# Kernel optimization log

Hardware: AMD Instinct MI355X
Metric: run time of the kernel (lower is better)

## Reference

```python
import jax, jax.numpy as jnp
import numpy as np

N, T, H = 307, 256, 64
NH, DH = 4, 16  # transformer heads, head dim (64/4)


def _layernorm(x, g, b, eps=1e-5):
    mu = x.mean(-1, keepdims=True)
    var = ((x - mu) ** 2).mean(-1, keepdims=True)
    return (x - mu) / jnp.sqrt(var + eps) * g + b


def _run_cell(x, m, tf, tj, Anorm, W0, b0, W1, mixW, mixb, Wih, Whh, bih, bhh, outW, outb, jamW, jamb):
    # x,m,tf,tj: [N,T]. Per-timestep 4-path ChebConv(K=2) + softmax mixing + GRUCell.
    hidden = Whh.shape[1]

    def step(h, xs):
        x_t, m_t, tf_t, tj_t = xs  # each [N]
        msg_in = jnp.concatenate([h, m_t[:, None], tf_t[:, None], tj_t[:, None]], axis=-1)  # [N,H+3]
        am = Anorm @ msg_in  # [N,H+3]
        m_all = jnp.tanh(jnp.einsum('ni,poi->npo', msg_in, W0) + b0
                         + jnp.einsum('ni,poi->npo', am, W1))  # [N,4,H]
        mix = jax.nn.softmax(h @ mixW.T + mixb, axis=1)  # [N,4]
        msg = jnp.einsum('np,npo->no', mix, m_all)  # [N,H]
        inp = jnp.concatenate([msg, (x_t * m_t)[:, None], m_t[:, None]], axis=-1)  # [N,H+2]
        # PyTorch GRUCell (gate order r,z,n)
        gi = inp @ Wih.T + bih
        gh = h @ Whh.T + bhh
        i_r, i_z, i_n = jnp.split(gi, 3, axis=-1)
        h_r, h_z, h_n = jnp.split(gh, 3, axis=-1)
        r = jax.nn.sigmoid(i_r + h_r)
        z = jax.nn.sigmoid(i_z + h_z)
        n = jnp.tanh(i_n + r * h_n)
        h_new = (1.0 - z) * n + z * h
        h2 = h_new + 0.1 * h
        pred = (h2 @ outW.T + outb)[:, 0]
        jam = (h2 @ jamW.T + jamb)[:, 0]
        return h2, (pred, jam, h2)

    h0 = jnp.zeros((x.shape[0], hidden), x.dtype)
    _, (preds, jams, hs) = jax.lax.scan(step, h0, (x.T, m.T, tf.T, tj.T))
    return preds.T, jams.T, jnp.transpose(hs, (1, 0, 2))  # [N,T],[N,T],[N,T,H]


def _pos_enc(Tlen, hdim, dtype):
    pos = jnp.arange(Tlen, dtype=dtype)[:, None]
    div = 10000.0 ** (jnp.arange(0, hdim, 2, dtype=dtype) / hdim)
    pe = jnp.zeros((Tlen, hdim), dtype)
    pe = pe.at[:, 0::2].set(jnp.sin(pos / div))
    pe = pe.at[:, 1::2].set(jnp.cos(pos / div))
    return pe


def _enhancer(h, qkvW, qkvb, oW, ob, g1, be1, f1W, f1b, f2W, f2b, g2, be2, pW, pb):
    # h: [N,T,H]; post-norm TransformerEncoder (relu, no dropout at eval), then Linear(H,1)
    x = h + _pos_enc(h.shape[1], h.shape[2], h.dtype)[None]
    n_layers = qkvW.shape[0]
    for l in range(n_layers):
        qkv = x @ qkvW[l].T + qkvb[l]
        q, k, v = jnp.split(qkv, 3, axis=-1)
        sh = (x.shape[0], x.shape[1], NH, DH)
        q, k, v = q.reshape(sh), k.reshape(sh), v.reshape(sh)
        att = jax.nn.softmax(jnp.einsum('nqhd,nkhd->nhqk', q, k) / np.sqrt(DH).astype(np.float32), axis=-1)
        o = jnp.einsum('nhqk,nkhd->nqhd', att, v).reshape(x.shape)
        o = o @ oW[l].T + ob[l]
        x = _layernorm(x + o, g1[l], be1[l])
        f = jax.nn.relu(x @ f1W[l].T + f1b[l]) @ f2W[l].T + f2b[l]
        x = _layernorm(x + f, g2[l], be2[l])
    return (x @ pW.T + pb)[..., 0]  # [N,T]


def _forward(x_seq, m_seq, tod_free, tod_jam, Anorm,
             cell_chebW0, cell_chebb0, cell_chebW1, cell_mixW, cell_mixb,
             cell_Wih, cell_Whh, cell_bih, cell_bhh,
             cell_outW, cell_outb, cell_jamW, cell_jamb,
             fuse_W1, fuse_b1, fuse_W2, fuse_b2,
             tr_qkvW, tr_qkvb, tr_oW, tr_ob, tr_ln1g, tr_ln1b,
             tr_ff1W, tr_ff1b, tr_ff2W, tr_ff2b, tr_ln2g, tr_ln2b,
             tr_projW, tr_projb):
    def cell(i, x, m, tf, tj):
        return _run_cell(x, m, tf, tj, Anorm,
                         cell_chebW0[i], cell_chebb0[i], cell_chebW1[i],
                         cell_mixW[i], cell_mixb[i],
                         cell_Wih[i], cell_Whh[i], cell_bih[i], cell_bhh[i],
                         cell_outW[i], cell_outb[i], cell_jamW[i], cell_jamb[i])

    flip = lambda a: a[:, ::-1]
    pf, jf, h_fwd = cell(0, x_seq, m_seq, tod_free, tod_jam)
    pb_r, jb_r, h_bwd_r = cell(1, flip(x_seq), flip(m_seq), flip(tod_free), flip(tod_jam))
    pb, jb, h_bwd = flip(pb_r), flip(jb_r), h_bwd_r[:, ::-1]

    fuse_in = jnp.stack([pf, pb], axis=-1)  # [N,T,2]
    w = jax.nn.softmax(jax.nn.relu(fuse_in @ fuse_W1.T + fuse_b1) @ fuse_W2.T + fuse_b2, axis=-1)
    speed = w[..., 0] * pf + w[..., 1] * pb
    jam_logit = w[..., 0] * jf + w[..., 1] * jb

    h_fused = h_fwd * w[..., 0:1] + h_bwd * w[..., 1:2]  # [N,T,H]
    args = lambda i: (tr_qkvW[i], tr_qkvb[i], tr_oW[i], tr_ob[i], tr_ln1g[i], tr_ln1b[i],
                      tr_ff1W[i], tr_ff1b[i], tr_ff2W[i], tr_ff2b[i], tr_ln2g[i], tr_ln2b[i],
                      tr_projW[i], tr_projb[i])
    speed_refined = _enhancer(h_fused, *args(0))
    jam_refined = _enhancer(h_fused, *args(1))
    alpha = 0.3
    speed = (1.0 - alpha) * speed + alpha * speed_refined
    jam_logit = (1.0 - alpha) * jam_logit + alpha * jam_refined
    return speed, jam_logit


def setup_inputs() -> dict:
    key = jax.random.key(0)
    keys = list(jax.random.split(key, 40))
    kit = iter(keys)

    def rn(shape, s=0.05):
        return s * jax.random.normal(next(kit), shape, jnp.float32)

    # sparse gaussian-normalized adjacency -> row-normalized diffusion matrix
    rng = np.random.default_rng(0)
    d = rng.uniform(0.5, 3.0, (N, N)); d = (d + d.T) / 2
    keep = rng.uniform(size=(N, N)) < 0.05; keep = keep | keep.T
    d = np.where(keep, d, np.inf)
    sigma = d[d < np.inf].std() + 1e-8
    adj = np.where(d < np.inf, np.exp(-d ** 2 / sigma ** 2), 0.0)
    np.fill_diagonal(adj, 1.0)
    dinv = np.where(adj.sum(1) > 0, (adj.sum(1) + 1e-8) ** -0.5, 0.0)
    adj_sym = adj * dinv[:, None] * dinv[None, :]
    rowsum = adj_sym.sum(1)
    Anorm = (adj_sym * np.where(rowsum > 0, 1.0 / rowsum, 0.0)[:, None]).astype(np.float32)

    inp = {
        'x_seq': jax.random.normal(next(kit), (N, T), jnp.float32),
        'm_seq': (jax.random.uniform(next(kit), (N, T)) < 0.5).astype(jnp.float32),
        'tod_free': jax.random.uniform(next(kit), (N, T), jnp.float32),
        'tod_jam': jax.random.uniform(next(kit), (N, T), jnp.float32),
        'Anorm': jnp.asarray(Anorm),
        'cell_chebW0': rn((2, 4, H, H + 3)), 'cell_chebb0': jnp.zeros((2, 4, H), jnp.float32),
        'cell_chebW1': rn((2, 4, H, H + 3)),
        'cell_mixW': rn((2, 4, H)), 'cell_mixb': jnp.zeros((2, 4), jnp.float32),
        'cell_Wih': rn((2, 3 * H, H + 2)), 'cell_Whh': rn((2, 3 * H, H)),
        'cell_bih': jnp.zeros((2, 3 * H), jnp.float32), 'cell_bhh': jnp.zeros((2, 3 * H), jnp.float32),
        'cell_outW': rn((2, 1, H)), 'cell_outb': jnp.zeros((2, 1), jnp.float32),
        'cell_jamW': rn((2, 1, H)), 'cell_jamb': jnp.zeros((2, 1), jnp.float32),
        'fuse_W1': rn((H, 2)), 'fuse_b1': jnp.zeros((H,), jnp.float32),
        'fuse_W2': rn((2, H)), 'fuse_b2': jnp.zeros((2,), jnp.float32),
        'tr_qkvW': rn((2, 3, 3 * H, H)), 'tr_qkvb': jnp.zeros((2, 3, 3 * H), jnp.float32),
        'tr_oW': rn((2, 3, H, H)), 'tr_ob': jnp.zeros((2, 3, H), jnp.float32),
        'tr_ln1g': jnp.ones((2, 3, H), jnp.float32), 'tr_ln1b': jnp.zeros((2, 3, H), jnp.float32),
        'tr_ff1W': rn((2, 3, 256, H)), 'tr_ff1b': jnp.zeros((2, 3, 256), jnp.float32),
        'tr_ff2W': rn((2, 3, H, 256)), 'tr_ff2b': jnp.zeros((2, 3, H), jnp.float32),
        'tr_ln2g': jnp.ones((2, 3, H), jnp.float32), 'tr_ln2b': jnp.zeros((2, 3, H), jnp.float32),
        'tr_projW': rn((2, 1, H)), 'tr_projb': jnp.zeros((2, 1), jnp.float32),
    }
    return inp


def reference(x_seq, m_seq, tod_free, tod_jam, Anorm,
              cell_chebW0, cell_chebb0, cell_chebW1, cell_mixW, cell_mixb,
              cell_Wih, cell_Whh, cell_bih, cell_bhh,
              cell_outW, cell_outb, cell_jamW, cell_jamb,
              fuse_W1, fuse_b1, fuse_W2, fuse_b2,
              tr_qkvW, tr_qkvb, tr_oW, tr_ob, tr_ln1g, tr_ln1b,
              tr_ff1W, tr_ff1b, tr_ff2W, tr_ff2b, tr_ln2g, tr_ln2b,
              tr_projW, tr_projb):
    return _forward(x_seq, m_seq, tod_free, tod_jam, Anorm,
                    cell_chebW0, cell_chebb0, cell_chebW1, cell_mixW, cell_mixb,
                    cell_Wih, cell_Whh, cell_bih, cell_bhh,
                    cell_outW, cell_outb, cell_jamW, cell_jamb,
                    fuse_W1, fuse_b1, fuse_W2, fuse_b2,
                    tr_qkvW, tr_qkvb, tr_oW, tr_ob, tr_ln1g, tr_ln1b,
                    tr_ff1W, tr_ff1b, tr_ff2W, tr_ff2b, tr_ln2g, tr_ln2b,
                    tr_projW, tr_projb)
```

## Files before the change

### kernel.cpp

```cpp
#include <hip/hip_runtime.h>
#include <math.h>

#define NN   307
#define TT   256
#define HHH  64
#define NROW (NN*TT)
#define NBLK_D 77
#define SCANB  154

#define OFF_O  (6*192*64)
#define OFF_F1 (OFF_O + 6*64*64)
#define OFF_F2 (OFF_F1 + 6*256*64)
#define NWTOT  (OFF_F2 + 6*64*256)

typedef unsigned short u16;
typedef __attribute__((ext_vector_type(8))) short short8;
typedef __attribute__((ext_vector_type(4))) float f4;

__device__ __forceinline__ float wsum(float v){
#pragma unroll
  for (int off = 32; off > 0; off >>= 1) v += __shfl_xor(v, off, 64);
  return v;
}
__device__ __forceinline__ float wsum16(float v){
#pragma unroll
  for (int off = 8; off > 0; off >>= 1) v += __shfl_xor(v, off, 64);
  return v;
}
__device__ __forceinline__ float ftanh(float x){
  x = fminf(20.f, fmaxf(-20.f, x));
  float e = __expf(2.f*x);
  return (e - 1.f)/(e + 1.f);
}
__device__ __forceinline__ float fsigm(float x){ return 1.f/(1.f + __expf(-x)); }

__device__ __forceinline__ u16 f2bf(float x){
  unsigned u = __float_as_uint(x);
  u += 0x7fffu + ((u >> 16) & 1u);
  return (u16)(u >> 16);
}
__device__ __forceinline__ float bf2f(u16 h){
  return __uint_as_float((unsigned)h << 16);
}
__device__ __forceinline__ void split8(const float* xv, short8& hi, short8& lo){
  union { short8 v; u16 u[8]; } H, L;
#pragma unroll
  for (int j = 0; j < 8; j++){
    const float x = xv[j];
    const u16 h = f2bf(x);
    H.u[j] = h;
    L.u[j] = f2bf(x - bf2f(h));
  }
  hi = H.v; lo = L.v;
}

__global__ void k_sparse(const float* __restrict__ A, int* __restrict__ cnt,
                         int* __restrict__ idx, float* __restrict__ val){
  int n = blockIdx.x*64 + threadIdx.x;
  if (n >= NN) return;
  int c = 0;
  for (int m = 0; m < NN; m++){
    float a = A[n*NN + m];
    if (a != 0.f){ idx[n*NN + c] = m; val[n*NN + c] = a; c++; }
  }
  cnt[n] = c;
}

__global__ void k_tr_cheb(const float* __restrict__ W0, const float* __restrict__ W1,
                          float* __restrict__ W0T, float* __restrict__ W1T){
  int t = blockIdx.x*256 + threadIdx.x;
  if (t >= 2*67*256) return;
  int c = t & 255; int rest = t >> 8; int i = rest % 67; int d = rest / 67;
  int p = c >> 6, o = c & 63;
  int src = ((d*4 + p)*64 + o)*67 + i;
  W0T[t] = W0[src];
  W1T[t] = W1[src];
}

__global__ void k_tr_gru(const float* __restrict__ Wih, const float* __restrict__ Whh,
                         float* __restrict__ WihT, float* __restrict__ WhhT){
  int t = blockIdx.x*256 + threadIdx.x;
  if (t < 2*66*192){
    int j = t % 192; int rest = t / 192; int i = rest % 66; int d = rest / 66;
    WihT[t] = Wih[(d*192 + j)*66 + i];
  }
  if (t < 2*64*192){
    int j = t % 192; int rest = t / 192; int i = rest % 64; int d = rest / 64;
    WhhT[t] = Whh[(d*192 + j)*64 + i];
  }
}

__global__ void k_af(const float* __restrict__ mseq, const float* __restrict__ tfr,
                     const float* __restrict__ tjm, const int* __restrict__ cnt,
                     const int* __restrict__ idx, const float* __restrict__ val,
                     float* __restrict__ AF){
  int n = blockIdx.x, c = blockIdx.y, t = threadIdx.x;
  const float* feat = (c == 0) ? mseq : (c == 1) ? tfr : tjm;
  float acc = 0.f; int k = cnt[n];
  for (int s = 0; s < k; s++) acc += val[n*NN + s] * feat[idx[n*NN + s]*TT + t];
  AF[((size_t)c*NN + n)*TT + t] = acc;
}

__global__ void k_split(const float* __restrict__ src, u16* __restrict__ hi,
                        u16* __restrict__ lo, int n){
  int i = blockIdx.x*256 + threadIdx.x;
  if (i >= n) return;
  const float x = src[i];
  const u16 h = f2bf(x);
  hi[i] = h;
  lo[i] = f2bf(x - bf2f(h));
}

__global__ __launch_bounds__(256, 1)
void k_scan(const float* __restrict__ xseq, const float* __restrict__ mseq,
            const float* __restrict__ tfr, const float* __restrict__ tjm,
            const float* __restrict__ W0T, const float* __restrict__ W1T,
            const float* __restrict__ b0g,
            const float* __restrict__ mixW, const float* __restrict__ mixb,
            const float* __restrict__ WihT, const float* __restrict__ WhhT,
            const float* __restrict__ bih, const float* __restrict__ bhh,
            const int* __restrict__ spcnt, const int* __restrict__ spidx,
            const float* __restrict__ spval, const float* __restrict__ AF,
            float* __restrict__ Hseq, int* __restrict__ slots)
{
  const int tid = threadIdx.x;
  const int bid = blockIdx.x;
  const int d   = bid / NBLK_D;
  const int n0  = (bid % NBLK_D) * 4;
  const int lane = tid & 63;
  const int wid  = tid >> 6;

  __shared__ __align__(16) float hsT[64][4];
  __shared__ __align__(16) float amsT[68][4];
  __shared__ __align__(16) float msgsT[64][4];
  __shared__ float malls[256][5];
  __shared__ float gis[4][192];
  __shared__ float ghs[4][192];
  __shared__ float mixs[4][4];
  __shared__ float xss[4], mss[4], tfs[4], tjs[4];
  __shared__ int   s_idx[4][320];
  __shared__ float s_val[4][320];
  __shared__ int   s_cnt[4];
  __shared__ int   s_need[NBLK_D];

  float w0r[67], w1r[67];
#pragma unroll
  for (int i = 0; i < 67; i++){
    w0r[i] = W0T[(d*67 + i)*256 + tid];
    w1r[i] = W1T[(d*67 + i)*256 + tid];
  }
  const float b0r = b0g[d*256 + tid];
  float wih_r[64], whh_r[64];
  float wih64 = 0.f, wih65 = 0.f, bih_r = 0.f, bhh_r = 0.f;
  if (tid < 192){
#pragma unroll
    for (int i = 0; i < 64; i++){
      whh_r[i] = WhhT[(d*64 + i)*192 + tid];
      wih_r[i] = WihT[(d*66 + i)*192 + tid];
    }
    wih64 = WihT[(d*66 + 64)*192 + tid];
    wih65 = WihT[(d*66 + 65)*192 + tid];
    bih_r = bih[d*192 + tid];
    bhh_r = bhh[d*192 + tid];
  }
  float mixw_r[4];
#pragma unroll
  for (int p = 0; p < 4; p++) mixw_r[p] = mixW[(d*4 + p)*64 + lane];
  const float mixb0 = mixb[d*4+0], mixb1 = mixb[d*4+1], mixb2 = mixb[d*4+2], mixb3 = mixb[d*4+3];

  for (int i = tid; i < NBLK_D; i += 256) s_need[i] = 0;
  __syncthreads();
  for (int r = 0; r < 4; r++){
    const int n = min(n0 + r, NN-1);
    const int cc = spcnt[n];
    const int ccp = (cc + 15) & ~15;
    if (tid == 0) s_cnt[r] = ccp;
    for (int s = tid; s < ccp; s += 256){
      const int m = (s < cc) ? spidx[n*NN + s] : 0;
      s_idx[r][s] = m;
      s_val[r][s] = (s < cc) ? spval[n*NN + s] : 0.f;
      s_need[m >> 2] = 1;
    }
  }
  hsT[lane][wid] = 0.f;
  __syncthreads();
  const bool need0 = (lane < NBLK_D) && (s_need[lane] != 0);
  const bool need1 = (lane + 64 < NBLK_D) && (s_need[lane + 64] != 0);

#pragma unroll 1
  for (int k = 0; k < TT; k++){
    const int ts = (d == 0) ? k : (TT-1 - k);
    if (tid < 4){
      const int r = tid; const int n = min(n0 + r, NN-1);
      const float mv = mseq[n*TT + ts];
      mss[r] = mv; tfs[r] = tfr[n*TT + ts]; tjs[r] = tjm[n*TT + ts];
      xss[r] = xseq[n*TT + ts];
      amsT[64][r] = AF[(0*NN + n)*TT + ts];
      amsT[65][r] = AF[(1*NN + n)*TT + ts];
      amsT[66][r] = AF[(2*NN + n)*TT + ts];
    }
    {
      const int r = wid;
      const float hv = hsT[lane][r];
      float l0 = wsum(hv * mixw_r[0]) + mixb0;
      float l1 = wsum(hv * mixw_r[1]) + mixb1;
      float l2 = wsum(hv * mixw_r[2]) + mixb2;
      float l3 = wsum(hv * mixw_r[3]) + mixb3;
      const float mx = fmaxf(fmaxf(l0,l1), fmaxf(l2,l3));
      const float e0 = __expf(l0-mx), e1 = __expf(l1-mx), e2 = __expf(l2-mx), e3 = __expf(l3-mx);
      const float inv = 1.f/(e0+e1+e2+e3);
      if (lane == 0){
        mixs[0][r] = e0*inv; mixs[1][r] = e1*inv; mixs[2][r] = e2*inv; mixs[3][r] = e3*inv;
      }
    }
    __syncthreads();
    {
      float a0 = b0r, a1 = b0r, a2 = b0r, a3 = b0r;
#pragma unroll
      for (int i = 0; i < 64; i++){
        const float4 h4 = *(const float4*)&hsT[i][0];
        const float w = w0r[i];
        a0 += h4.x*w; a1 += h4.y*w; a2 += h4.z*w; a3 += h4.w*w;
      }
      a0 += mss[0]*w0r[64] + tfs[0]*w0r[65] + tjs[0]*w0r[66];
      a1 += mss[1]*w0r[64] + tfs[1]*w0r[65] + tjs[1]*w0r[66];
      a2 += mss[2]*w0r[64] + tfs[2]*w0r[65] + tjs[2]*w0r[66];
      a3 += mss[3]*w0r[64] + tfs[3]*w0r[65] + tjs[3]*w0r[66];
      malls[tid][0] = a0; malls[tid][1] = a1; malls[tid][2] = a2; malls[tid][3] = a3;
    }
    if (tid < 192){
      float g0 = bhh_r, g1 = bhh_r, g2 = bhh_r, g3 = bhh_r;
#pragma unroll
      for (int i = 0; i < 64; i++){
        const float4 h4 = *(const float4*)&hsT[i][0];
        const float w = whh_r[i];
        g0 += h4.x*w; g1 += h4.y*w; g2 += h4.z*w; g3 += h4.w*w;
      }
      ghs[0][tid] = g0; ghs[1][tid] = g1; ghs[2][tid] = g2; ghs[3][tid] = g3;
      gis[0][tid] = bih_r + (xss[0]*mss[0])*wih64 + mss[0]*wih65;
      gis[1][tid] = bih_r + (xss[1]*mss[1])*wih64 + mss[1]*wih65;
      gis[2][tid] = bih_r + (xss[2]*mss[2])*wih64 + mss[2]*wih65;
      gis[3][tid] = bih_r + (xss[3]*mss[3])*wih64 + mss[3]*wih65;
    }
    if (k > 0 && tid < 64){
      const int* sl = slots + (size_t)d*NBLK_D*16;
      for (;;){
        const int va = need0
            ? __hip_atomic_load(&sl[lane*16], __ATOMIC_RELAXED, __HIP_MEMORY_SCOPE_AGENT)
            : 0x7fffffff;
        const int vb = need1
            ? __hip_atomic_load(&sl[(lane+64)*16], __ATOMIC_RELAXED, __HIP_MEMORY_SCOPE_AGENT)
            : 0x7fffffff;
        if (__all(min(va, vb) >= k)) break;
        __builtin_amdgcn_s_sleep(1);
      }
    }
    __syncthreads();
    {
      const float* Hprev = Hseq + (size_t)(d*257 + k)*NN*64;
      const int r = wid;
      const int ccp = s_cnt[r];
      float acc = 0.f;
      for (int s = 0; s < ccp; s += 16){
        float aV[16], hV[16];
#pragma unroll
        for (int u = 0; u < 16; u++){
          const int m = s_idx[r][s+u];
          aV[u] = s_val[r][s+u];
          hV[u] = __hip_atomic_load(&Hprev[(size_t)m*64 + lane],
                                    __ATOMIC_RELAXED, __HIP_MEMORY_SCOPE_AGENT);
        }
#pragma unroll
        for (int u = 0; u < 16; u++) acc += aV[u]*hV[u];
      }
      amsT[lane][r] = acc;
    }
    __syncthreads();
    {
      const int p = tid >> 6;
      float pa0 = malls[tid][0], pa1 = malls[tid][1], pa2 = malls[tid][2], pa3 = malls[tid][3];
#pragma unroll
      for (int i = 0; i < 67; i++){
        const float4 m4 = *(const float4*)&amsT[i][0];
        const float w = w1r[i];
        pa0 += m4.x*w; pa1 += m4.y*w; pa2 += m4.z*w; pa3 += m4.w*w;
      }
      malls[tid][0] = mixs[p][0]*ftanh(pa0);
      malls[tid][1] = mixs[p][1]*ftanh(pa1);
      malls[tid][2] = mixs[p][2]*ftanh(pa2);
      malls[tid][3] = mixs[p][3]*ftanh(pa3);
    }
    __syncthreads();
    msgsT[lane][wid] = malls[lane][wid] + malls[64+lane][wid] + malls[128+lane][wid] + malls[192+lane][wid];
    __syncthreads();
    if (tid < 192){
      float q0 = gis[0][tid], q1 = gis[1][tid], q2 = gis[2][tid], q3 = gis[3][tid];
#pragma unroll
      for (int i = 0; i < 64; i++){
        const float4 m4 = *(const float4*)&msgsT[i][0];
        const float w = wih_r[i];
        q0 += m4.x*w; q1 += m4.y*w; q2 += m4.z*w; q3 += m4.w*w;
      }
      gis[0][tid] = q0; gis[1][tid] = q1; gis[2][tid] = q2; gis[3][tid] = q3;
    }
    __syncthreads();
    {
      const int r = wid, o = lane;
      const float ir = gis[r][o], iz = gis[r][o+64], in_ = gis[r][o+128];
      const float hr = ghs[r][o], hz = ghs[r][o+64], hn = ghs[r][o+128];
      const float rr2 = fsigm(ir + hr);
      const float zz = fsigm(iz + hz);
      const float nnv = ftanh(in_ + rr2*hn);
      const float hold = hsT[o][r];
      const float h2 = (1.f - zz)*nnv + zz*hold + 0.1f*hold;
      hsT[o][r] = h2;
      const int n = n0 + r;
      if (n < NN)
        __hip_atomic_store(&Hseq[((size_t)(d*257 + k + 1)*NN + n)*64 + o], h2,
                           __ATOMIC_RELAXED, __HIP_MEMORY_SCOPE_AGENT);
    }
    __syncthreads();
    if (tid == 0)
      __hip_atomic_store(&slots[bid*16], k + 1, __ATOMIC_RELAXED, __HIP_MEMORY_SCOPE_AGENT);
  }
}

__global__ __launch_bounds__(256)
void k_fusion(const float* __restrict__ Hseq,
              const float* __restrict__ outW, const float* __restrict__ outb,
              const float* __restrict__ jamW, const float* __restrict__ jamb,
              const float* __restrict__ fw1, const float* __restrict__ fb1,
              const float* __restrict__ fw2, const float* __restrict__ fb2,
              float* __restrict__ x0, float* __restrict__ outp)
{
  const int tid = threadIdx.x;
  const int rr = tid >> 6, lane = tid & 63;
  const int idx = blockIdx.x*4 + rr;
  const int n = idx >> 8, t = idx & 255;
  const float hf = Hseq[((size_t)(0*257 + t + 1)*NN + n)*64 + lane];
  const float hb = Hseq[((size_t)(257 + 256 - t)*NN + n)*64 + lane];
  const float pf = wsum(hf * outW[lane])      + outb[0];
  const float pb = wsum(hb * outW[64 + lane]) + outb[1];
  const float jf = wsum(hf * jamW[lane])      + jamb[0];
  const float jb = wsum(hb * jamW[64 + lane]) + jamb[1];
  const float hid = fmaxf(fw1[lane*2]*pf + fw1[lane*2+1]*pb + fb1[lane], 0.f);
  const float l0 = wsum(hid * fw2[lane]) + fb2[0];
  const float l1 = wsum(hid * fw2[64+lane]) + fb2[1];
  const float mx = fmaxf(l0,l1);
  const float e0 = __expf(l0-mx), e1 = __expf(l1-mx);
  const float inv = 1.f/(e0+e1);
  const float w0 = e0*inv, w1 = e1*inv;
  const int i2 = lane & ~1;
  const float dv = powf(10000.f, (float)i2 * (1.f/64.f));
  const float arg = (float)t / dv;
  const float pe = (lane & 1) ? cosf(arg) : sinf(arg);
  x0[(size_t)idx*64 + lane] = hf*w0 + hb*w1 + pe;
  if (lane == 0){
    outp[idx]        = 0.7f*(w0*pf + w1*pb);
    outp[NROW + idx] = 0.7f*(w0*jf + w1*jb);
  }
}

__global__ __launch_bounds__(256)
void k_qkattn(const float* __restrict__ X0, const float* __restrict__ XBUF, int lyr,
              const u16* __restrict__ WHI, const u16* __restrict__ WLO,
              const float* __restrict__ qkvb_all, float* __restrict__ OBUF)
{
  __shared__ __align__(16) u16 Xhi[256][72];
  __shared__ __align__(16) u16 Vt [4][16][280];
  __shared__ __align__(16) u16 Pst[4][16][264];
  __shared__ __align__(16) u16 Kscr[4][16][24];
  __shared__ __align__(16) u16 Qhs[4][16][24];
  __shared__ __align__(16) u16 Qls[4][16][24];
  const int n = blockIdx.x;
  const int e = blockIdx.y;
  const int el = e*3 + lyr;
  const float* X = (lyr == 0) ? X0 : (XBUF + (size_t)e*NROW*64);
  const u16* Whi = WHI + (size_t)el*192*64;
  const u16* Wlo = WLO + (size_t)el*192*64;
  const float* bias = qkvb_all + (size_t)el*192;
  float* O = OBUF + (size_t)e*NROW*64;
  const int tid = threadIdx.x;
  const int h = tid >> 6;
  const int l = tid & 63;
  const int m16 = l & 15, q = l >> 4;
  const float* xbase = X + (size_t)n*256*64;
  const short8 z8 = {0,0,0,0,0,0,0,0};

  {
    const float* xr = xbase + (size_t)tid*64;
#pragma unroll
    for (int c = 0; c < 64; c += 8){
      float v[8];
      *(float4*)&v[0] = *(const float4*)&xr[c];
      *(float4*)&v[4] = *(const float4*)&xr[c+4];
      union { short8 s; u16 u[8]; } pk;
#pragma unroll
      for (int j = 0; j < 8; j++) pk.u[j] = f2bf(v[j]);
      *(short8*)&Xhi[tid][c] = pk.s;
    }
  }
  __syncthreads();

  short8 WqH[2], WqL[2], WkH[2], WkL[2], WvH[2], WvL[2];
#pragma unroll
  for (int kh = 0; kh < 2; kh++){
    const size_t rq = (size_t)(h*16 + m16)*64 + kh*32 + q*8;
    const size_t rk = (size_t)(64 + h*16 + m16)*64 + kh*32 + q*8;
    const size_t rv = (size_t)(128 + h*16 + m16)*64 + kh*32 + q*8;
    WqH[kh] = *(const short8*)&Whi[rq]; WqL[kh] = *(const short8*)&Wlo[rq];
    WkH[kh] = *(const short8*)&Whi[rk]; WkL[kh] = *(const short8*)&Wlo[rk];
    WvH[kh] = *(const short8*)&Whi[rv]; WvL[kh] = *(const short8*)&Wlo[rv];
  }
  const float qb = bias[h*16 + m16];
  const float kb = bias[64 + h*16 + m16];
  const float vb = bias[128 + h*16 + m16];

  short8 Kb[16];
#pragma unroll 1
  for (int ct = 0; ct < 16; ct++){
    short8 Xa0 = *(const short8*)&Xhi[ct*16 + m16][q*8];
    short8 Xa1 = *(const short8*)&Xhi[ct*16 + m16][32 + q*8];
    f4 ka = {0.f,0.f,0.f,0.f}, va = {0.f,0.f,0.f,0.f};
    ka = __builtin_amdgcn_mfma_f32_16x16x32_bf16(Xa0, WkH[0], ka, 0, 0, 0);
    ka = __builtin_amdgcn_mfma_f32_16x16x32_bf16(Xa0, WkL[0], ka, 0, 0, 0);
    ka = __builtin_amdgcn_mfma_f32_16x16x32_bf16(Xa1, WkH[1], ka, 0, 0, 0);
    ka = __builtin_amdgcn_mfma_f32_16x16x32_bf16(Xa1, WkL[1], ka, 0, 0, 0);
    va = __builtin_amdgcn_mfma_f32_16x16x32_bf16(Xa0, WvH[0], va, 0, 0, 0);
    va = __builtin_amdgcn_mfma_f32_16x16x32_bf16(Xa0, WvL[0], va, 0, 0, 0);
    va = __builtin_amdgcn_mfma_f32_16x16x32_bf16(Xa1, WvH[1], va, 0, 0, 0);
    va = __builtin_amdgcn_mfma_f32_16x16x32_bf16(Xa1, WvL[1], va, 0, 0, 0);
#pragma unroll
    for (int r = 0; r < 4; r++){
      Kscr[h][q*4 + r][m16] = f2bf(ka[r] + kb);
      Vt[h][m16][ct*16 + q*4 + r] = f2bf(va[r] + vb);
    }
    Kb[ct] = (q < 2) ? *(const short8*)&Kscr[h][m16][q*8] : z8;
  }

#pragma unroll 1
  for (int c = 0; c < 16; c++){
    short8 Xa0 = *(const short8*)&Xhi[c*16 + m16][q*8];
    short8 Xa1 = *(const short8*)&Xhi[c*16 + m16][32 + q*8];
    f4 qa = {0.f,0.f,0.f,0.f};
    qa = __builtin_amdgcn_mfma_f32_16x16x32_bf16(Xa0, WqH[0], qa, 0, 0, 0);
    qa = __builtin_amdgcn_mfma_f32_16x16x32_bf16(Xa0, WqL[0], qa, 0, 0, 0);
    qa = __builtin_amdgcn_mfma_f32_16x16x32_bf16(Xa1, WqH[1], qa, 0, 0, 0);
    qa = __builtin_amdgcn_mfma_f32_16x16x32_bf16(Xa1, WqL[1], qa, 0, 0, 0);
#pragma unroll
    for (int r = 0; r < 4; r++){
      const float qv = (qa[r] + qb) * 0.25f;
      const u16 hh = f2bf(qv);
      Qhs[h][q*4 + r][m16] = hh;
      Qls[h][q*4 + r][m16] = f2bf(qv - bf2f(hh));
    }
    short8 Qh = z8, Ql = z8;
    if (q < 2){
      Qh = *(const short8*)&Qhs[h][m16][q*8];
      Ql = *(const short8*)&Qls[h][m16][q*8];
    }
    float rs[4] = {0.f, 0.f, 0.f, 0.f};
#pragma unroll
    for (int ct = 0; ct < 16; ct++){
      f4 s = {0.f,0.f,0.f,0.f};
      s = __builtin_amdgcn_mfma_f32_16x16x32_bf16(Qh, Kb[ct], s, 0, 0, 0);
      s = __builtin_amdgcn_mfma_f32_16x16x32_bf16(Ql, Kb[ct], s, 0, 0, 0);
#pragma unroll
      for (int r = 0; r < 4; r++){
        const float p = __expf(s[r]);
        rs[r] += p;
        Pst[h][q*4 + r][ct*16 + m16] = f2bf(p);
      }
    }
#pragma unroll
    for (int r = 0; r < 4; r++) rs[r] = wsum16(rs[r]);
    f4 acc = {0.f,0.f,0.f,0.f};
#pragma unroll
    for (int kt = 0; kt < 8; kt++){
      const short8 Pa = *(const short8*)&Pst[h][m16][kt*32 + q*8];
      const short8 Vb = *(const short8*)&Vt[h][m16][kt*32 + q*8];
      acc = __builtin_amdgcn_mfma_f32_16x16x32_bf16(Pa, Vb, acc, 0, 0, 0);
    }
#pragma unroll
    for (int r = 0; r < 4; r++){
      O[((size_t)n*256 + c*16 + q*4 + r)*64 + h*16 + m16] = acc[r] / rs[r];
    }
  }
}

__global__ __launch_bounds__(256)
void k_oproj_ln(const float* __restrict__ OBUF, const float* __restrict__ X0,
                float* __restrict__ XBUF, int lyr,
                const u16* __restrict__ WHI, const u16* __restrict__ WLO,
                const float* __restrict__ ob_all,
                const float* __restrict__ g_all, const float* __restrict__ b_all)
{
  const int e = blockIdx.y;
  const int el = e*3 + lyr;
  const float* X = OBUF + (size_t)e*NROW*64;
  const float* Xres = (lyr == 0) ? X0 : (XBUF + (size_t)e*NROW*64);
  float* Y = XBUF + (size_t)e*NROW*64;
  const u16* Whi = WHI + OFF_O + (size_t)el*64*64;
  const u16* Wlo = WLO + OFF_O + (size_t)el*64*64;
  const float* bias = ob_all + (size_t)el*64;
  const float* g = g_all + (size_t)el*64;
  const float* b = b_all + (size_t)el*64;
  const int tid = threadIdx.x;
  const int w = tid >> 6, l = tid & 63;
  const int m16 = l & 15, q = l >> 4;
  const int row = blockIdx.x*64 + w*16 + m16;
  short8 Ah[2], Al[2];
#pragma unroll
  for (int kh = 0; kh < 2; kh++){
    float xv[8];
    *(float4*)&xv[0] = *(const float4*)&X[(size_t)row*64 + kh*32 + q*8];
    *(float4*)&xv[4] = *(const float4*)&X[(size_t)row*64 + kh*32 + q*8 + 4];
    split8(xv, Ah[kh], Al[kh]);
  }
  f4 acc[4];
#pragma unroll
  for (int nt = 0; nt < 4; nt++){
    acc[nt] = (f4){0.f, 0.f, 0.f, 0.f};
    const int n = nt*16 + m16;
#pragma unroll
    for (int kh = 0; kh < 2; kh++){
      const short8 Bh = *(const short8*)&Whi[(size_t)n*64 + kh*32 + q*8];
      const short8 Bl = *(const short8*)&Wlo[(size_t)n*64 + kh*32 + q*8];
      acc[nt] = __builtin_amdgcn_mfma_f32_16x16x32_bf16(Ah[kh], Bh, acc[nt], 0, 0, 0);
      acc[nt] = __builtin_amdgcn_mfma_f32_16x16x32_bf16(Ah[kh], Bl, acc[nt], 0, 0, 0);
      acc[nt] = __builtin_amdgcn_mfma_f32_16x16x32_bf16(Al[kh], Bh, acc[nt], 0, 0, 0);
    }
  }
  const int rbase = blockIdx.x*64 + w*16 + q*4;
#pragma unroll
  for (int r = 0; r < 4; r++){
    float v[4]; float s = 0.f;
#pragma unroll
    for (int nt = 0; nt < 4; nt++){
      const int col = nt*16 + m16;
      v[nt] = acc[nt][r] + bias[col] + Xres[(size_t)(rbase + r)*64 + col];
      s += v[nt];
    }
    const float mu = wsum16(s) * (1.f/64.f);
    float vs = 0.f;
#pragma unroll
    for (int nt = 0; nt < 4; nt++){ v[nt] -= mu; vs += v[nt]*v[nt]; }
    const float rstd = rsqrtf(wsum16(vs) * (1.f/64.f) + 1e-5f);
#pragma unroll
    for (int nt = 0; nt < 4; nt++){
      const int col = nt*16 + m16;
      Y[(size_t)(rbase + r)*64 + col] = v[nt] * rstd * g[col] + b[col];
    }
  }
}

__global__ __launch_bounds__(256)
void k_ffblock(float* __restrict__ XBUF, int lyr,
               const u16* __restrict__ WHI, const u16* __restrict__ WLO,
               const float* __restrict__ b1_all, const float* __restrict__ b2_all,
               const float* __restrict__ g_all, const float* __restrict__ b_all)
{
  __shared__ __align__(16) u16 Hs[64][280];
  const int e = blockIdx.y;
  const int el = e*3 + lyr;
  float* X = XBUF + (size_t)e*NROW*64;
  const u16* W1hi = WHI + OFF_F1 + (size_t)el*256*64;
  const u16* W1lo = WLO + OFF_F1 + (size_t)el*256*64;
  const u16* W2hi = WHI + OFF_F2 + (size_t)el*64*256;
  const u16* W2lo = WLO + OFF_F2 + (size_t)el*64*256;
  const float* b1 = b1_all + (size_t)el*256;
  const float* b2 = b2_all + (size_t)el*64;
  const float* g = g_all + (size_t)el*64;
  const float* b = b_all + (size_t)el*64;
  const int tid = threadIdx.x;
  const int w = tid >> 6, l = tid & 63;
  const int m16 = l & 15, q = l >> 4;
  const int row = blockIdx.x*64 + w*16 + m16;
  short8 Ah[2], Al[2];
#pragma unroll
  for (int kh = 0; kh < 2; kh++){
    float xv[8];
    *(float4*)&xv[0] = *(const float4*)&X[(size_t)row*64 + kh*32 + q*8];
    *(float4*)&xv[4] = *(const float4*)&X[(size_t)row*64 + kh*32 + q*8 + 4];
    split8(xv, Ah[kh], Al[kh]);
  }
  for (int nt = 0; nt < 16; nt++){
    const int n = nt*16 + m16;
    f4 acc = {0.f, 0.f, 0.f, 0.f};
#pragma unroll
    for (int kh = 0; kh < 2; kh++){
      const short8 Bh = *(const short8*)&W1hi[(size_t)n*64 + kh*32 + q*8];
      const short8 Bl = *(const short8*)&W1lo[(size_t)n*64 + kh*32 + q*8];
      acc = __builtin_amdgcn_mfma_f32_16x16x32_bf16(Ah[kh], Bh, acc, 0, 0, 0);
      acc = __builtin_amdgcn_mfma_f32_16x16x32_bf16(Ah[kh], Bl, acc, 0, 0, 0);
      acc = __builtin_amdgcn_mfma_f32_16x16x32_bf16(Al[kh], Bh, acc, 0, 0, 0);
    }
    const float bb = b1[n];
#pragma unroll
    for (int r = 0; r < 4; r++){
      const float h = fmaxf(acc[r] + bb, 0.f);
      Hs[w*16 + q*4 + r][n] = f2bf(h);
    }
  }
  __syncthreads();
  f4 acc2[4];
#pragma unroll
  for (int nt = 0; nt < 4; nt++) acc2[nt] = (f4){0.f, 0.f, 0.f, 0.f};
#pragma unroll 1
  for (int kh = 0; kh < 8; kh++){
    const short8 Ahh = *(const short8*)&Hs[w*16 + m16][kh*32 + q*8];
#pragma unroll
    for (int nt = 0; nt < 4; nt++){
      const int n = nt*16 + m16;
      const short8 Bh = *(const short8*)&W2hi[(size_t)n*256 + kh*32 + q*8];
      const short8 Bl = *(const short8*)&W2lo[(size_t)n*256 + kh*32 + q*8];
      acc2[nt] = __builtin_amdgcn_mfma_f32_16x16x32_bf16(Ahh, Bh, acc2[nt], 0, 0, 0);
      acc2[nt] = __builtin_amdgcn_mfma_f32_16x16x32_bf16(Ahh, Bl, acc2[nt], 0, 0, 0);
    }
  }
  const int rbase = blockIdx.x*64 + w*16 + q*4;
#pragma unroll
  for (int r = 0; r < 4; r++){
    float v[4]; float s = 0.f;
#pragma unroll
    for (int nt = 0; nt < 4; nt++){
      const int col = nt*16 + m16;
      v[nt] = acc2[nt][r] + b2[col] + X[(size_t)(rbase + r)*64 + col];
      s += v[nt];
    }
    const float mu = wsum16(s) * (1.f/64.f);
    float vs = 0.f;
#pragma unroll
    for (int nt = 0; nt < 4; nt++){ v[nt] -= mu; vs += v[nt]*v[nt]; }
    const float rstd = rsqrtf(wsum16(vs) * (1.f/64.f) + 1e-5f);
#pragma unroll
    for (int nt = 0; nt < 4; nt++){
      const int col = nt*16 + m16;
      X[(size_t)(rbase + r)*64 + col] = v[nt] * rstd * g[col] + b[col];
    }
  }
}

__global__ __launch_bounds__(256)
void k_proj_add(const float* __restrict__ XBUF, const float* __restrict__ prW,
                const float* __restrict__ prb, float* __restrict__ out)
{
  const int e = blockIdx.y;
  const float* X = XBUF + (size_t)e*NROW*64;
  const float* pW = prW + (size_t)e*64;
  float* outp = out + (size_t)e*NROW;
  const int tid = threadIdx.x;
  const int r = tid >> 6, lane = tid & 63;
  const size_t row = (size_t)blockIdx.x*4 + r;
  const float v = X[row*64 + lane] * pW[lane];
  const float s = wsum(v);
  if (lane == 0) outp[row] += 0.3f*(s + prb[e]);
}

extern "C" void kernel_launch(void* const* d_in, const int* in_sizes, int n_in,
                              void* d_out, int out_size, void* d_ws, size_t ws_size,
                              hipStream_t stream)
{
  const float* x_seq = (const float*)d_in[0];
  const float* m_seq = (const float*)d_in[1];
  const float* tod_f = (const float*)d_in[2];
  const float* tod_j = (const float*)d_in[3];
  const float* Anorm = (const float*)d_in[4];
  const float* chW0  = (const float*)d_in[5];
  const float* chb0  = (const float*)d_in[6];
  const float* chW1  = (const float*)d_in[7];
  const float* mixW  = (const float*)d_in[8];
  const float* mixb  = (const float*)d_in[9];
  const float* Wih   = (const float*)d_in[10];
  const float* Whh   = (const float*)d_in[11];
  const float* bih   = (const float*)d_in[12];
  const float* bhh   = (const float*)d_in[13];
  const float* outW  = (const float*)d_in[14];
  const float* outbp = (const float*)d_in[15];
  const float* jamW  = (const float*)d_in[16];
  const float* jambp = (const float*)d_in[17];
  const float* fW1   = (const float*)d_in[18];
  const float* fb1   = (const float*)d_in[19];
  const float* fW2   = (const float*)d_in[20];
  const float* fb2   = (const float*)d_in[21];
  const float* qkvW  = (const float*)d_in[22];
  const float* qkvb  = (const float*)d_in[23];
  const float* oW    = (const float*)d_in[24];
  const float* ob    = (const float*)d_in[25];
  const float* ln1g  = (const float*)d_in[26];
  const float* ln1b  = (const float*)d_in[27];
  const float* f1W   = (const float*)d_in[28];
  const float* f1b   = (const float*)d_in[29];
  const float* f2W   = (const float*)d_in[30];
  const float* f2b   = (const float*)d_in[31];
  const float* ln2g  = (const float*)d_in[32];
  const float* ln2b  = (const float*)d_in[33];
  const float* prW   = (const float*)d_in[34];
  const float* prb   = (const float*)d_in[35];
  float* out = (float*)d_out;

  float* ws = (float*)d_ws;
  size_t off = 0;
  auto take = [&](size_t n)->float*{ float* p = ws + off; off += (n + 63) & ~(size_t)63; return p; };
  int*   slots = (int*)take(4096);
  float* W0T  = take((size_t)2*67*256);
  float* W1T  = take((size_t)2*67*256);
  float* WihT = take((size_t)2*66*192);
  float* WhhT = take((size_t)2*64*192);
  int*   spcnt = (int*)take(320);
  int*   spidx = (int*)take((size_t)NN*NN);
  float* spval = take((size_t)NN*NN);
  float* AF    = take((size_t)3*NN*TT);
  float* HSEQ  = take((size_t)2*257*NN*64);
  float* X0    = take((size_t)NROW*64);
  float* XBUF  = take((size_t)2*NROW*64);
  float* OBUF  = take((size_t)2*NROW*64);
  u16* WHI = (u16*)take(((size_t)NWTOT + 1)/2);
  u16* WLO = (u16*)take(((size_t)NWTOT + 1)/2);
  (void)ws_size; (void)in_sizes; (void)n_in; (void)out_size;

  const size_t NQKV = (size_t)6*192*64;
  const size_t NO   = (size_t)6*64*64;
  const size_t NF1  = (size_t)6*256*64;
  const size_t NF2  = (size_t)6*64*256;

  hipMemsetAsync(slots, 0, 4096*sizeof(int), stream);
  hipMemsetAsync(HSEQ, 0, (size_t)NN*64*sizeof(float), stream);
  hipMemsetAsync(HSEQ + (size_t)257*NN*64, 0, (size_t)NN*64*sizeof(float), stream);

  k_sparse<<<dim3((NN+63)/64), dim3(64), 0, stream>>>(Anorm, spcnt, spidx, spval);
  k_tr_cheb<<<dim3(134), dim3(256), 0, stream>>>(chW0, chW1, W0T, W1T);
  k_tr_gru<<<dim3(99), dim3(256), 0, stream>>>(Wih, Whh, WihT, WhhT);
  k_af<<<dim3(NN,3), dim3(256), 0, stream>>>(m_seq, tod_f, tod_j, spcnt, spidx, spval, AF);
  k_split<<<dim3((int)((NQKV+255)/256)), dim3(256), 0, stream>>>(qkvW, WHI, WLO, (int)NQKV);
  k_split<<<dim3((int)((NO+255)/256)), dim3(256), 0, stream>>>(oW, WHI+OFF_O, WLO+OFF_O, (int)NO);
  k_split<<<dim3((int)((NF1+255)/256)), dim3(256), 0, stream>>>(f1W, WHI+OFF_F1, WLO+OFF_F1, (int)NF1);
  k_split<<<dim3((int)((NF2+255)/256)), dim3(256), 0, stream>>>(f2W, WHI+OFF_F2, WLO+OFF_F2, (int)NF2);

  k_scan<<<dim3(SCANB), dim3(256), 0, stream>>>(x_seq, m_seq, tod_f, tod_j, W0T, W1T,
      chb0, mixW, mixb, WihT, WhhT, bih, bhh,
      spcnt, spidx, spval, AF, HSEQ, slots);

  k_fusion<<<dim3(NROW/4), dim3(256), 0, stream>>>(HSEQ, outW, outbp, jamW, jambp,
      fW1, fb1, fW2, fb2, X0, out);

  for (int l = 0; l < 3; l++){
    k_qkattn<<<dim3(NN, 2), dim3(256), 0, stream>>>(X0, XBUF, l, WHI, WLO, qkvb, OBUF);
    k_oproj_ln<<<dim3(NROW/64, 2), dim3(256), 0, stream>>>(OBUF, X0, XBUF, l,
        WHI, WLO, ob, ln1g, ln1b);
    k_ffblock<<<dim3(NROW/64, 2), dim3(256), 0, stream>>>(XBUF, l, WHI, WLO,
        f1b, f2b, ln2g, ln2b);
  }
  k_proj_add<<<dim3(NROW/4, 2), dim3(256), 0, stream>>>(XBUF, prW, prb, out);
}
```

Baseline: 4.352 ms.

## Fuse out-projection LayerNorm with FFN block and drop attention X staging

Merges the attention output projection plus first LayerNorm with the feed-forward block and second LayerNorm into one kernel. The normalized activations stay in registers and shared memory, so the intermediate write and read of XBUF and one launch per layer go away. Separately, the attention kernel now reads X rows straight from global memory inside the K/V and Q loops instead of staging a bf16 copy in shared memory, which frees LDS and removes a barrier. In exchange, each X row is loaded from global twice. The fused kernel also uses more shared memory and registers, which may lower occupancy.

```diff
diff --git a/kernel.cpp b/kernel.cpp
--- a/kernel.cpp
+++ b/kernel.cpp
@@ -52,6 +52,12 @@
     L.u[j] = f2bf(x - bf2f(h));
   }
   hi = H.v; lo = L.v;
+}
+__device__ __forceinline__ short8 pack_hi8(const float* xv){
+  union { short8 s; u16 u[8]; } pk;
+#pragma unroll
+  for (int j = 0; j < 8; j++) pk.u[j] = f2bf(xv[j]);
+  return pk.s;
 }
 
 __global__ void k_sparse(const float* __restrict__ A, int* __restrict__ cnt,
@@ -366,7 +372,6 @@
               const u16* __restrict__ WHI, const u16* __restrict__ WLO,
               const float* __restrict__ qkvb_all, float* __restrict__ OBUF)
 {
-  __shared__ __align__(16) u16 Xhi[256][72];
   __shared__ __align__(16) u16 Vt [4][16][280];
   __shared__ __align__(16) u16 Pst[4][16][264];
   __shared__ __align__(16) u16 Kscr[4][16][24];
@@ -387,21 +392,6 @@
   const float* xbase = X + (size_t)n*256*64;
   const short8 z8 = {0,0,0,0,0,0,0,0};
 
-  {
-    const float* xr = xbase + (size_t)tid*64;
-#pragma unroll
-    for (int c = 0; c < 64; c += 8){
-      float v[8];
-      *(float4*)&v[0] = *(const float4*)&xr[c];
-      *(float4*)&v[4] = *(const float4*)&xr[c+4];
-      union { short8 s; u16 u[8]; } pk;
-#pragma unroll
-      for (int j = 0; j < 8; j++) pk.u[j] = f2bf(v[j]);
-      *(short8*)&Xhi[tid][c] = pk.s;
-    }
-  }
-  __syncthreads();
-
   short8 WqH[2], WqL[2], WkH[2], WkL[2], WvH[2], WvL[2];
 #pragma unroll
   for (int kh = 0; kh < 2; kh++){
@@ -419,8 +409,14 @@
   short8 Kb[16];
 #pragma unroll 1
   for (int ct = 0; ct < 16; ct++){
-    short8 Xa0 = *(const short8*)&Xhi[ct*16 + m16][q*8];
-    short8 Xa1 = *(const short8*)&Xhi[ct*16 + m16][32 + q*8];
+    const float* xr = xbase + (size_t)(ct*16 + m16)*64;
+    float xv0[8], xv1[8];
+    *(float4*)&xv0[0] = *(const float4*)&xr[q*8];
+    *(float4*)&xv0[4] = *(const float4*)&xr[q*8 + 4];
+    *(float4*)&xv1[0] = *(const float4*)&xr[32 + q*8];
+    *(float4*)&xv1[4] = *(const float4*)&xr[32 + q*8 + 4];
+    const short8 Xa0 = pack_hi8(xv0);
+    const short8 Xa1 = pack_hi8(xv1);
     f4 ka = {0.f,0.f,0.f,0.f}, va = {0.f,0.f,0.f,0.f};
     ka = __builtin_amdgcn_mfma_f32_16x16x32_bf16(Xa0, WkH[0], ka, 0, 0, 0);
     ka = __builtin_amdgcn_mfma_f32_16x16x32_bf16(Xa0, WkL[0], ka, 0, 0, 0);
@@ -440,8 +436,14 @@
 
 #pragma unroll 1
   for (int c = 0; c < 16; c++){
-    short8 Xa0 = *(const short8*)&Xhi[c*16 + m16][q*8];
-    short8 Xa1 = *(const short8*)&Xhi[c*16 + m16][32 + q*8];
+    const float* xr = xbase + (size_t)(c*16 + m16)*64;
+    float xv0[8], xv1[8];
+    *(float4*)&xv0[0] = *(const float4*)&xr[q*8];
+    *(float4*)&xv0[4] = *(const float4*)&xr[q*8 + 4];
+    *(float4*)&xv1[0] = *(const float4*)&xr[32 + q*8];
+    *(float4*)&xv1[4] = *(const float4*)&xr[32 + q*8 + 4];
+    const short8 Xa0 = pack_hi8(xv0);
+    const short8 Xa1 = pack_hi8(xv1);
     f4 qa = {0.f,0.f,0.f,0.f};
     qa = __builtin_amdgcn_mfma_f32_16x16x32_bf16(Xa0, WqH[0], qa, 0, 0, 0);
     qa = __builtin_amdgcn_mfma_f32_16x16x32_bf16(Xa0, WqL[0], qa, 0, 0, 0);
@@ -489,32 +491,47 @@
 }
 
 __global__ __launch_bounds__(256)
-void k_oproj_ln(const float* __restrict__ OBUF, const float* __restrict__ X0,
-                float* __restrict__ XBUF, int lyr,
-                const u16* __restrict__ WHI, const u16* __restrict__ WLO,
-                const float* __restrict__ ob_all,
-                const float* __restrict__ g_all, const float* __restrict__ b_all)
+void k_mlp(const float* __restrict__ OBUF, const float* __restrict__ X0,
+           float* __restrict__ XBUF, int lyr,
+           const u16* __restrict__ WHI, const u16* __restrict__ WLO,
+           const float* __restrict__ ob_all,
+           const float* __restrict__ g1_all, const float* __restrict__ b1ln_all,
+           const float* __restrict__ f1b_all, const float* __restrict__ f2b_all,
+           const float* __restrict__ g2_all, const float* __restrict__ b2ln_all)
 {
+  __shared__ __align__(16) u16 Xh[64][72];
+  __shared__ __align__(16) u16 Xl[64][72];
+  __shared__ __align__(16) u16 Hs[64][280];
   const int e = blockIdx.y;
   const int el = e*3 + lyr;
-  const float* X = OBUF + (size_t)e*NROW*64;
+  const float* Oin = OBUF + (size_t)e*NROW*64;
   const float* Xres = (lyr == 0) ? X0 : (XBUF + (size_t)e*NROW*64);
   float* Y = XBUF + (size_t)e*NROW*64;
-  const u16* Whi = WHI + OFF_O + (size_t)el*64*64;
-  const u16* Wlo = WLO + OFF_O + (size_t)el*64*64;
-  const float* bias = ob_all + (size_t)el*64;
-  const float* g = g_all + (size_t)el*64;
-  const float* b = b_all + (size_t)el*64;
+  const u16* oWhi = WHI + OFF_O + (size_t)el*64*64;
+  const u16* oWlo = WLO + OFF_O + (size_t)el*64*64;
+  const u16* W1hi = WHI + OFF_F1 + (size_t)el*256*64;
+  const u16* W1lo = WLO + OFF_F1 + (size_t)el*256*64;
+  const u16* W2hi = WHI + OFF_F2 + (size_t)el*64*256;
+  const u16* W2lo = WLO + OFF_F2 + (size_t)el*64*256;
+  const float* obb = ob_all + (size_t)el*64;
+  const float* g1 = g1_all + (size_t)el*64;
+  const float* b1ln = b1ln_all + (size_t)el*64;
+  const float* f1b = f1b_all + (size_t)el*256;
+  const float* f2b = f2b_all + (size_t)el*64;
+  const float* g2 = g2_all + (size_t)el*64;
+  const float* b2ln = b2ln_all + (size_t)el*64;
   const int tid = threadIdx.x;
   const int w = tid >> 6, l = tid & 63;
   const int m16 = l & 15, q = l >> 4;
   const int row = blockIdx.x*64 + w*16 + m16;
+  const int rbase = blockIdx.x*64 + w*16 + q*4;
+
   short8 Ah[2], Al[2];
 #pragma unroll
   for (int kh = 0; kh < 2; kh++){
     float xv[8];
-    *(float4*)&xv[0] = *(const float4*)&X[(size_t)row*64 + kh*32 + q*8];
-    *(float4*)&xv[4] = *(const float4*)&X[(size_t)row*64 + kh*32 + q*8 + 4];
+    *(float4*)&xv[0] = *(const float4*)&Oin[(size_t)row*64 + kh*32 + q*8];
+    *(float4*)&xv[4] = *(const float4*)&Oin[(size_t)row*64 + kh*32 + q*8 + 4];
     split8(xv, Ah[kh], Al[kh]);
   }
   f4 acc[4];
@@ -524,85 +541,61 @@
     const int n = nt*16 + m16;
 #pragma unroll
     for (int kh = 0; kh < 2; kh++){
-      const short8 Bh = *(const short8*)&Whi[(size_t)n*64 + kh*32 + q*8];
-      const short8 Bl = *(const short8*)&Wlo[(size_t)n*64 + kh*32 + q*8];
+      const short8 Bh = *(const short8*)&oWhi[(size_t)n*64 + kh*32 + q*8];
+      const short8 Bl = *(const short8*)&oWlo[(size_t)n*64 + kh*32 + q*8];
       acc[nt] = __builtin_amdgcn_mfma_f32_16x16x32_bf16(Ah[kh], Bh, acc[nt], 0, 0, 0);
       acc[nt] = __builtin_amdgcn_mfma_f32_16x16x32_bf16(Ah[kh], Bl, acc[nt], 0, 0, 0);
       acc[nt] = __builtin_amdgcn_mfma_f32_16x16x32_bf16(Al[kh], Bh, acc[nt], 0, 0, 0);
     }
   }
-  const int rbase = blockIdx.x*64 + w*16 + q*4;
+  float vv[4][4];
 #pragma unroll
   for (int r = 0; r < 4; r++){
-    float v[4]; float s = 0.f;
+    float s = 0.f;
 #pragma unroll
     for (int nt = 0; nt < 4; nt++){
       const int col = nt*16 + m16;
-      v[nt] = acc[nt][r] + bias[col] + Xres[(size_t)(rbase + r)*64 + col];
-      s += v[nt];
+      vv[r][nt] = acc[nt][r] + obb[col] + Xres[(size_t)(rbase + r)*64 + col];
+      s += vv[r][nt];
     }
     const float mu = wsum16(s) * (1.f/64.f);
     float vs = 0.f;
 #pragma unroll
-    for (int nt = 0; nt < 4; nt++){ v[nt] -= mu; vs += v[nt]*v[nt]; }
+    for (int nt = 0; nt < 4; nt++){ vv[r][nt] -= mu; vs += vv[r][nt]*vv[r][nt]; }
     const float rstd = rsqrtf(wsum16(vs) * (1.f/64.f) + 1e-5f);
 #pragma unroll
     for (int nt = 0; nt < 4; nt++){
       const int col = nt*16 + m16;
-      Y[(size_t)(rbase + r)*64 + col] = v[nt] * rstd * g[col] + b[col];
-    }
-  }
-}
-
-__global__ __launch_bounds__(256)
-void k_ffblock(float* __restrict__ XBUF, int lyr,
-               const u16* __restrict__ WHI, const u16* __restrict__ WLO,
-               const float* __restrict__ b1_all, const float* __restrict__ b2_all,
-               const float* __restrict__ g_all, const float* __restrict__ b_all)
-{
-  __shared__ __align__(16) u16 Hs[64][280];
-  const int e = blockIdx.y;
-  const int el = e*3 + lyr;
-  float* X = XBUF + (size_t)e*NROW*64;
-  const u16* W1hi = WHI + OFF_F1 + (size_t)el*256*64;
-  const u16* W1lo = WLO + OFF_F1 + (size_t)el*256*64;
-  const u16* W2hi = WHI + OFF_F2 + (size_t)el*64*256;
-  const u16* W2lo = WLO + OFF_F2 + (size_t)el*64*256;
-  const float* b1 = b1_all + (size_t)el*256;
-  const float* b2 = b2_all + (size_t)el*64;
-  const float* g = g_all + (size_t)el*64;
-  const float* b = b_all + (size_t)el*64;
-  const int tid = threadIdx.x;
-  const int w = tid >> 6, l = tid & 63;
-  const int m16 = l & 15, q = l >> 4;
-  const int row = blockIdx.x*64 + w*16 + m16;
-  short8 Ah[2], Al[2];
+      vv[r][nt] = vv[r][nt] * rstd * g1[col] + b1ln[col];
+      const u16 hh = f2bf(vv[r][nt]);
+      Xh[w*16 + q*4 + r][col] = hh;
+      Xl[w*16 + q*4 + r][col] = f2bf(vv[r][nt] - bf2f(hh));
+    }
+  }
+  short8 Xa_h[2], Xa_l[2];
 #pragma unroll
   for (int kh = 0; kh < 2; kh++){
-    float xv[8];
-    *(float4*)&xv[0] = *(const float4*)&X[(size_t)row*64 + kh*32 + q*8];
-    *(float4*)&xv[4] = *(const float4*)&X[(size_t)row*64 + kh*32 + q*8 + 4];
-    split8(xv, Ah[kh], Al[kh]);
+    Xa_h[kh] = *(const short8*)&Xh[w*16 + m16][kh*32 + q*8];
+    Xa_l[kh] = *(const short8*)&Xl[w*16 + m16][kh*32 + q*8];
   }
   for (int nt = 0; nt < 16; nt++){
     const int n = nt*16 + m16;
-    f4 acc = {0.f, 0.f, 0.f, 0.f};
+    f4 a1 = {0.f, 0.f, 0.f, 0.f};
 #pragma unroll
     for (int kh = 0; kh < 2; kh++){
       const short8 Bh = *(const short8*)&W1hi[(size_t)n*64 + kh*32 + q*8];
       const short8 Bl = *(const short8*)&W1lo[(size_t)n*64 + kh*32 + q*8];
-      acc = __builtin_amdgcn_mfma_f32_16x16x32_bf16(Ah[kh], Bh, acc, 0, 0, 0);
-      acc = __builtin_amdgcn_mfma_f32_16x16x32_bf16(Ah[kh], Bl, acc, 0, 0, 0);
-      acc = __builtin_amdgcn_mfma_f32_16x16x32_bf16(Al[kh], Bh, acc, 0, 0, 0);
-    }
-    const float bb = b1[n];
+      a1 = __builtin_amdgcn_mfma_f32_16x16x32_bf16(Xa_h[kh], Bh, a1, 0, 0, 0);
+      a1 = __builtin_amdgcn_mfma_f32_16x16x32_bf16(Xa_h[kh], Bl, a1, 0, 0, 0);
+      a1 = __builtin_amdgcn_mfma_f32_16x16x32_bf16(Xa_l[kh], Bh, a1, 0, 0, 0);
+    }
+    const float bb = f1b[n];
 #pragma unroll
     for (int r = 0; r < 4; r++){
-      const float h = fmaxf(acc[r] + bb, 0.f);
+      const float h = fmaxf(a1[r] + bb, 0.f);
       Hs[w*16 + q*4 + r][n] = f2bf(h);
     }
   }
-  __syncthreads();
   f4 acc2[4];
 #pragma unroll
   for (int nt = 0; nt < 4; nt++) acc2[nt] = (f4){0.f, 0.f, 0.f, 0.f};
@@ -618,14 +611,13 @@
       acc2[nt] = __builtin_amdgcn_mfma_f32_16x16x32_bf16(Ahh, Bl, acc2[nt], 0, 0, 0);
     }
   }
-  const int rbase = blockIdx.x*64 + w*16 + q*4;
 #pragma unroll
   for (int r = 0; r < 4; r++){
     float v[4]; float s = 0.f;
 #pragma unroll
     for (int nt = 0; nt < 4; nt++){
       const int col = nt*16 + m16;
-      v[nt] = acc2[nt][r] + b2[col] + X[(size_t)(rbase + r)*64 + col];
+      v[nt] = acc2[nt][r] + f2b[col] + vv[r][nt];
       s += v[nt];
     }
     const float mu = wsum16(s) * (1.f/64.f);
@@ -636,7 +628,7 @@
 #pragma unroll
     for (int nt = 0; nt < 4; nt++){
       const int col = nt*16 + m16;
-      X[(size_t)(rbase + r)*64 + col] = v[nt] * rstd * g[col] + b[col];
+      Y[(size_t)(rbase + r)*64 + col] = v[nt] * rstd * g2[col] + b2ln[col];
     }
   }
 }
@@ -746,10 +738,8 @@
 
   for (int l = 0; l < 3; l++){
     k_qkattn<<<dim3(NN, 2), dim3(256), 0, stream>>>(X0, XBUF, l, WHI, WLO, qkvb, OBUF);
-    k_oproj_ln<<<dim3(NROW/64, 2), dim3(256), 0, stream>>>(OBUF, X0, XBUF, l,
-        WHI, WLO, ob, ln1g, ln1b);
-    k_ffblock<<<dim3(NROW/64, 2), dim3(256), 0, stream>>>(XBUF, l, WHI, WLO,
-        f1b, f2b, ln2g, ln2b);
+    k_mlp<<<dim3(NROW/64, 2), dim3(256), 0, stream>>>(OBUF, X0, XBUF, l,
+        WHI, WLO, ob, ln1g, ln1b, f1b, f2b, ln2g, ln2b);
   }
   k_proj_add<<<dim3(NROW/4, 2), dim3(256), 0, stream>>>(XBUF, prW, prb, out);
 }
```

Result: no change. 4.341 ms (-0.3%).
